# Kernel optimization log

Measured on AMD Instinct MI355X. Metric: run time of the kernel, lower is better.

Reference implementation:

```python
import math
import jax, jax.numpy as jnp
import numpy as np

N_EMBD = 1024
N_HEAD = 16
HEAD_DIM = N_EMBD // N_HEAD
B, T = 4, 2048
LN_EPS = 1e-5


def setup_inputs() -> dict:
    key = jax.random.key(0)
    ks = jax.random.split(key, 20)
    s = 0.02
    d = {
        'x': jax.random.normal(ks[0], (B, T, N_EMBD), jnp.float32),
        'Wq': jax.random.normal(ks[1], (N_EMBD, N_EMBD), jnp.float32) * s,
        'bq': jnp.zeros((N_EMBD,), jnp.float32),
        'Wk': jax.random.normal(ks[2], (N_EMBD, N_EMBD), jnp.float32) * s,
        'bk': jnp.zeros((N_EMBD,), jnp.float32),
        'Wv': jax.random.normal(ks[3], (N_EMBD, N_EMBD), jnp.float32) * s,
        'bv': jnp.zeros((N_EMBD,), jnp.float32),
        'Wo': jax.random.normal(ks[4], (N_EMBD, N_EMBD), jnp.float32) * s,
        'bo': jnp.zeros((N_EMBD,), jnp.float32),
        'ln1_g': jnp.ones((N_EMBD,), jnp.float32),
        'ln1_b': jnp.zeros((N_EMBD,), jnp.float32),
        'ln2_g': jnp.ones((N_EMBD,), jnp.float32),
        'ln2_b': jnp.zeros((N_EMBD,), jnp.float32),
        'W_fc': jax.random.normal(ks[5], (N_EMBD, 4 * N_EMBD), jnp.float32) * s,
        'b_fc': jnp.zeros((4 * N_EMBD,), jnp.float32),
        'W_proj': jax.random.normal(ks[6], (4 * N_EMBD, N_EMBD), jnp.float32) * s,
        'b_proj': jnp.zeros((N_EMBD,), jnp.float32),
    }
    return d


def _layernorm(x, g, b):
    mu = jnp.mean(x, axis=-1, keepdims=True)
    var = jnp.var(x, axis=-1, keepdims=True)
    return (x - mu) * jax.lax.rsqrt(var + LN_EPS) * g + b


def _new_gelu(x):
    c = math.sqrt(2.0 / math.pi)
    return 0.5 * x * (1.0 + jnp.tanh(c * (x + 0.044715 * x ** 3)))


def _attn(x, Wq, bq, Wk, bk, Wv, bv, Wo, bo):
    Bq, Tq, C = x.shape
    def heads(y):  # (B,T,C) -> (B,H,T,D)
        return y.reshape(Bq, Tq, N_HEAD, HEAD_DIM).transpose(0, 2, 1, 3)
    q = heads(x @ Wq + bq)
    k = heads(x @ Wk + bk)
    v = heads(x @ Wv + bv)
    scores = jnp.einsum('bhqd,bhkd->bhqk', q, k) / math.sqrt(HEAD_DIM)
    causal = jnp.tril(jnp.ones((Tq, Tq), bool))
    scores = jnp.where(causal, scores, -jnp.inf)
    w = jax.nn.softmax(scores, axis=-1)
    av = jnp.einsum('bhqk,bhkd->bhqd', w, v)
    av = av.transpose(0, 2, 1, 3).reshape(Bq, Tq, C)
    return av @ Wo + bo


def reference(x, Wq, bq, Wk, bk, Wv, bv, Wo, bo, ln1_g, ln1_b, ln2_g, ln2_b, W_fc, b_fc, W_proj, b_proj):
    x = x + _attn(_layernorm(x, ln1_g, ln1_b), Wq, bq, Wk, bk, Wv, bv, Wo, bo)
    h = _layernorm(x, ln2_g, ln2_b)
    x = x + (_new_gelu(h @ W_fc + b_fc) @ W_proj + b_proj)
    return x
```

## Files before the change

### kernel.cpp

```cpp
#include <hip/hip_runtime.h>

typedef __attribute__((ext_vector_type(8))) short short8;
typedef __attribute__((ext_vector_type(4))) short short4v;
typedef __attribute__((ext_vector_type(4))) float floatx4;
typedef unsigned short u16;

#define MFMA16(a,b,c) __builtin_amdgcn_mfma_f32_16x16x32_bf16(a,b,c,0,0,0)

typedef const __attribute__((address_space(1))) void* gas1;
typedef __attribute__((address_space(3))) void* las3;
static __device__ __forceinline__ void glds16(const void* g, void* l){
  __builtin_amdgcn_global_load_lds((gas1)g, (las3)l, 16, 0, 0);
}

static __device__ __forceinline__ u16 f2b(float f){
  union { float f; unsigned int u; } c; c.f = f;
  unsigned int u = c.u;
  u += 0x7fffu + ((u >> 16) & 1u);
  return (u16)(u >> 16);
}

static __device__ __forceinline__ unsigned int cvtpk(float lo, float hi){
  unsigned int r;
  asm("v_cvt_pk_bf16_f32 %0, %1, %2" : "=v"(r) : "v"(lo), "v"(hi));
  return r;
}

__global__ __launch_bounds__(256) void prep_kernel(
    const float* __restrict__ Wq, const float* __restrict__ Wk,
    const float* __restrict__ Wv, const float* __restrict__ Wo,
    const float* __restrict__ Wfc, const float* __restrict__ Wpj,
    u16* __restrict__ Wqkvt, u16* __restrict__ Wot,
    u16* __restrict__ Wfct, u16* __restrict__ Wpjt,
    const float* __restrict__ bq, const float* __restrict__ bk,
    const float* __restrict__ bv, float* __restrict__ bqkv)
{
  const int id = blockIdx.x;
  if (id == 12288){
    for (int i = threadIdx.x; i < 3072; i += 256)
      bqkv[i] = i < 1024 ? bq[i] : (i < 2048 ? bk[i - 1024] : bv[i - 2048]);
    return;
  }
  const float* W; u16* Wt; int K, N, loc, tshift;
  if (id < 4096){
    K = 1024; N = 1024; loc = id & 1023; tshift = 5;
    const int w = id >> 10;
    W  = (w == 0) ? Wq : (w == 1) ? Wk : (w == 2) ? Wv : Wo;
    Wt = (w == 3) ? Wot : Wqkvt + (size_t)w * 1024 * 1024;
  } else if (id < 8192){
    K = 1024; N = 4096; loc = id - 4096; tshift = 7; W = Wfc; Wt = Wfct;
  } else {
    K = 4096; N = 1024; loc = id - 8192; tshift = 5; W = Wpj; Wt = Wpjt;
  }
  const int nx = (loc & ((1 << tshift) - 1)) * 32;
  const int kx = (loc >> tshift) * 32;
  __shared__ float tile[32][33];
  const int tx = threadIdx.x & 31, ty = threadIdx.x >> 5;
  #pragma unroll
  for (int i = ty; i < 32; i += 8)
    tile[i][tx] = W[(size_t)(kx + i) * N + nx + tx];
  __syncthreads();
  #pragma unroll
  for (int i = ty; i < 32; i += 8)
    Wt[(size_t)(nx + i) * K + kx + tx] = f2b(tile[tx][i]);
}

__global__ __launch_bounds__(256) void ln_kernel(
    const float* __restrict__ x, const float* __restrict__ g,
    const float* __restrict__ b, u16* __restrict__ out){
  const int row = blockIdx.x, tid = threadIdx.x;
  const float4 v = reinterpret_cast<const float4*>(x + (size_t)row * 1024)[tid];
  float s  = v.x + v.y + v.z + v.w;
  float s2 = v.x*v.x + v.y*v.y + v.z*v.z + v.w*v.w;
  #pragma unroll
  for (int off = 1; off < 64; off <<= 1){
    s  += __shfl_xor(s,  off);
    s2 += __shfl_xor(s2, off);
  }
  __shared__ float red[8];
  const int wave = tid >> 6, lane = tid & 63;
  if (lane == 0){ red[wave] = s; red[4 + wave] = s2; }
  __syncthreads();
  s  = red[0] + red[1] + red[2] + red[3];
  s2 = red[4] + red[5] + red[6] + red[7];
  const float mu  = s * (1.f/1024.f);
  const float var = s2 * (1.f/1024.f) - mu * mu;
  const float rs  = rsqrtf(var + 1e-5f);
  const float4 gg = reinterpret_cast<const float4*>(g)[tid];
  const float4 bb = reinterpret_cast<const float4*>(b)[tid];
  ushort4 o;
  o.x = f2b((v.x - mu) * rs * gg.x + bb.x);
  o.y = f2b((v.y - mu) * rs * gg.y + bb.y);
  o.z = f2b((v.z - mu) * rs * gg.z + bb.z);
  o.w = f2b((v.w - mu) * rs * gg.w + bb.w);
  reinterpret_cast<ushort4*>(out + (size_t)row * 1024)[tid] = o;
}

template<bool GELU, bool RES, bool OUTBF, bool QKVMODE>
__global__ __launch_bounds__(256) void gemm128(
    const u16* __restrict__ A, const u16* __restrict__ Bt,
    const float* __restrict__ bias,
    const float* __restrict__ res,
    float* __restrict__ outF, u16* __restrict__ outB,
    u16* __restrict__ vtb,
    int M, int N, int K)
{
  __shared__ __attribute__((aligned(16))) u16 sA[2][128 * 32];
  __shared__ __attribute__((aligned(16))) u16 sB[2][128 * 32];
  const int tid  = threadIdx.x;
  const int wave = tid >> 6, lane = tid & 63, quad = lane >> 4, l16 = lane & 15;
  const int m0 = blockIdx.x * 128, n0 = blockIdx.y * 128;
  const int wm = (wave >> 1) * 64, wn = (wave & 1) * 64;

  const int scol = ((lane & 3) ^ ((lane >> 3) & 3)) * 8;
  const size_t aoff  = (size_t)(m0 + wave*32 + (lane >> 2)) * K + scol;
  const size_t aoff2 = aoff + (size_t)16 * K;
  const int brow = n0 + (wave >> 1)*64 + 4*(lane >> 2) + (wave & 1)*2;
  const size_t boff  = (size_t)brow * K + scol;
  const size_t boff2 = boff + (size_t)K;
  u16* alp = sA[0] + wave * 1024;
  u16* blp = sB[0] + wave * 1024;
  const int qx = (quad ^ ((l16 >> 1) & 3)) * 8;

  floatx4 acc[4][4];
  #pragma unroll
  for (int i = 0; i < 4; i++)
    #pragma unroll
    for (int nt = 0; nt < 4; nt++) acc[i][nt] = floatx4{0.f,0.f,0.f,0.f};

  glds16(A  + aoff,  alp);
  glds16(A  + aoff2, alp + 512);
  glds16(Bt + boff,  blp);
  glds16(Bt + boff2, blp + 512);

  int buf = 0;
  for (int k0 = 0; k0 < K; k0 += 32, buf ^= 1){
    __syncthreads();
    if (k0 + 32 < K){
      const int kn = k0 + 32;
      const int bo = (buf ^ 1) * 4096;
      glds16(A  + aoff  + kn, alp + bo);
      glds16(A  + aoff2 + kn, alp + bo + 512);
      glds16(Bt + boff  + kn, blp + bo);
      glds16(Bt + boff2 + kn, blp + bo + 512);
    }
    const u16* sa = sA[buf];
    const u16* sb = sB[buf];
    short8 af[4], bf[4];
    #pragma unroll
    for (int i = 0; i < 4; i++)
      af[i] = *reinterpret_cast<const short8*>(&sa[(wm + i*16 + l16)*32 + qx]);
    #pragma unroll
    for (int nt = 0; nt < 4; nt++)
      bf[nt] = *reinterpret_cast<const short8*>(&sb[(wn + nt*16 + l16)*32 + qx]);
    #pragma unroll
    for (int i = 0; i < 4; i++)
      #pragma unroll
      for (int nt = 0; nt < 4; nt++)
        acc[i][nt] = MFMA16(af[i], bf[nt], acc[i][nt]);
  }

  const int col0 = n0 + wn + 4*l16;
  const floatx4 bi = *reinterpret_cast<const floatx4*>(&bias[col0]);

  if (QKVMODE && n0 >= 2048){
    #pragma unroll
    for (int nt = 0; nt < 4; nt++){
      const int hd = col0 + nt - 2048;
      u16* vcol = vtb + (size_t)(hd >> 6) * 131072 + (size_t)(hd & 63) * 2048;
      #pragma unroll
      for (int i = 0; i < 4; i++){
        const int t0 = m0 + wm + i*16 + quad*4;
        const int bb = t0 >> 11, tt = t0 & 2047;
        short4v pk;
        #pragma unroll
        for (int r = 0; r < 4; r++) pk[r] = (short)f2b(acc[i][nt][r] + bi[nt]);
        *reinterpret_cast<short4v*>(vcol + (size_t)bb * 2097152 + tt) = pk;
      }
    }
    return;
  }

  #pragma unroll
  for (int i = 0; i < 4; i++){
    #pragma unroll
    for (int r = 0; r < 4; r++){
      const int row = m0 + wm + i*16 + quad*4 + r;
      if (OUTBF){
        short4v o;
        #pragma unroll
        for (int nt = 0; nt < 4; nt++){
          float val = acc[i][nt][r] + bi[nt];
          if (GELU){
            const float t = 0.7978845608028654f * (val + 0.044715f * val * val * val);
            val = val / (1.f + __expf(-2.f * t));
          }
          o[nt] = (short)f2b(val);
        }
        *reinterpret_cast<short4v*>(&outB[(size_t)row * N + col0]) = o;
      } else {
        floatx4 v;
        #pragma unroll
        for (int nt = 0; nt < 4; nt++) v[nt] = acc[i][nt][r] + bi[nt];
        if (RES){
          const floatx4 rr = *reinterpret_cast<const floatx4*>(&res[(size_t)row * N + col0]);
          #pragma unroll
          for (int nt = 0; nt < 4; nt++) v[nt] += rr[nt];
        }
        *reinterpret_cast<floatx4*>(&outF[(size_t)row * N + col0]) = v;
      }
    }
  }
}

__global__ __launch_bounds__(256) void attn_kernel(
    const u16* __restrict__ qkv, const u16* __restrict__ vtb,
    u16* __restrict__ O)
{
  constexpr int T = 2048, LDQ = 3072, LDP = 72;
  constexpr float CE = 0.18033688011112042f;
  __shared__ __attribute__((aligned(16))) u16 sK[2][2][64*32];
  __shared__ __attribute__((aligned(16))) u16 sV[2][2][64*32];
  __shared__ __attribute__((aligned(16))) u16 sP[4][16*LDP];

  const int tid = threadIdx.x, wave = tid >> 6, lane = tid & 63;
  const int quad = lane >> 4, l16 = lane & 15;

  const int lin = blockIdx.y * 16 + blockIdx.x;
  const int j = lin & 15;
  const int bh = lin >> 4;
  const int kk4 = bh >> 4;
  const int jj = (j + ((kk4 & 2) << 2)) & 15;
  const int qt = (kk4 & 1) ? (15 - jj) : jj;
  const int q0 = qt * 128;
  const int b = bh >> 4, h = bh & 15;

  const u16* Qp = qkv + (size_t)b * T * LDQ + h * 64;
  const u16* Kp = Qp + 1024;
  const u16* Vt = vtb + (size_t)bh * 64 * T;

  const int qx = (quad ^ ((l16 >> 1) & 3)) * 8;

  int qg[2]; qg[0] = q0 + wave*16 + l16; qg[1] = qg[0] + 64;
  short8 qf[2][2];
  #pragma unroll
  for (int g = 0; g < 2; g++){
    qf[g][0] = *reinterpret_cast<const short8*>(&Qp[(size_t)qg[g]*LDQ + quad*8]);
    qf[g][1] = *reinterpret_cast<const short8*>(&Qp[(size_t)qg[g]*LDQ + 32 + quad*8]);
  }

  float m_i[2] = {-INFINITY, -INFINITY}, l_i[2] = {0.f, 0.f};
  floatx4 o_acc[2][4];
  #pragma unroll
  for (int g = 0; g < 2; g++)
    #pragma unroll
    for (int nt = 0; nt < 4; nt++) o_acc[g][nt] = floatx4{0.f,0.f,0.f,0.f};

  const int srow = wave*16 + (lane >> 2);
  const int scol = ((lane & 3) ^ ((lane >> 3) & 3)) * 8;
  const int asrc = (lane & 48) | (quad * 4);

  const int kend = q0 + 128;

  {
    glds16(Kp + (size_t)srow*LDQ + scol,      sK[0][0] + wave*512);
    glds16(Kp + (size_t)srow*LDQ + 32 + scol, sK[0][1] + wave*512);
    glds16(Vt + (size_t)srow*T + scol,        sV[0][0] + wave*512);
    glds16(Vt + (size_t)srow*T + 32 + scol,   sV[0][1] + wave*512);
  }

  int buf = 0;
  for (int k0 = 0; k0 < kend; k0 += 64, buf ^= 1){
    __syncthreads();
    if (k0 + 64 < kend){
      const int kn = k0 + 64;
      glds16(Kp + (size_t)(kn + srow)*LDQ + scol,      sK[buf^1][0] + wave*512);
      glds16(Kp + (size_t)(kn + srow)*LDQ + 32 + scol, sK[buf^1][1] + wave*512);
      glds16(Vt + (size_t)srow*T + kn + scol,          sV[buf^1][0] + wave*512);
      glds16(Vt + (size_t)srow*T + kn + 32 + scol,     sV[buf^1][1] + wave*512);
    }

    #pragma unroll
    for (int g = 0; g < 2; g++){
      if (g == 0 && k0 > q0) continue;

      float s[4][4];
      __builtin_amdgcn_s_setprio(1);
      #pragma unroll
      for (int sub = 0; sub < 4; sub++){
        floatx4 sa = floatx4{0.f,0.f,0.f,0.f};
        const short8 kf0 = *reinterpret_cast<const short8*>(&sK[buf][0][(sub*16 + l16)*32 + qx]);
        const short8 kf1 = *reinterpret_cast<const short8*>(&sK[buf][1][(sub*16 + l16)*32 + qx]);
        sa = MFMA16(kf0, qf[g][0], sa);
        sa = MFMA16(kf1, qf[g][1], sa);
        #pragma unroll
        for (int r = 0; r < 4; r++) s[sub][r] = sa[r];
      }
      __builtin_amdgcn_s_setprio(0);
      if (k0 == q0 + g*64){
        #pragma unroll
        for (int sub = 0; sub < 4; sub++)
          #pragma unroll
          for (int r = 0; r < 4; r++){
            const int kidx = k0 + sub*16 + quad*4 + r;
            if (kidx > qg[g]) s[sub][r] = -1e30f;
          }
      }

      float sm[4];
      #pragma unroll
      for (int sub = 0; sub < 4; sub++)
        sm[sub] = fmaxf(fmaxf(s[sub][0], s[sub][1]), fmaxf(s[sub][2], s[sub][3]));
      float mx = fmaxf(fmaxf(sm[0], sm[1]), fmaxf(sm[2], sm[3]));
      mx = fmaxf(mx, __shfl_xor(mx, 16));
      mx = fmaxf(mx, __shfl_xor(mx, 32));

      const bool up = mx > m_i[g] + 32.f;
      const float mnew = up ? mx : m_i[g];

      float p[4][4], rs[4];
      #pragma unroll
      for (int sub = 0; sub < 4; sub++){
        #pragma unroll
        for (int r = 0; r < 4; r++)
          p[sub][r] = __builtin_amdgcn_exp2f(CE * (s[sub][r] - mnew));
        rs[sub] = (p[sub][0] + p[sub][1]) + (p[sub][2] + p[sub][3]);
      }
      float rowsum = (rs[0] + rs[1]) + (rs[2] + rs[3]);
      rowsum += __shfl_xor(rowsum, 16);
      rowsum += __shfl_xor(rowsum, 32);

      if (__any(up)){
        const float alpha = up ? __builtin_amdgcn_exp2f(CE * (m_i[g] - mnew)) : 1.f;
        float arow[4];
        #pragma unroll
        for (int r = 0; r < 4; r++) arow[r] = __shfl(alpha, asrc + r);
        #pragma unroll
        for (int nt = 0; nt < 4; nt++)
          #pragma unroll
          for (int r = 0; r < 4; r++) o_acc[g][nt][r] *= arow[r];
        l_i[g] *= alpha;
        m_i[g] = mnew;
      }
      l_i[g] += rowsum;

      #pragma unroll
      for (int sub = 0; sub < 4; sub++){
        uint2 pk2;
        pk2.x = cvtpk(p[sub][0], p[sub][1]);
        pk2.y = cvtpk(p[sub][2], p[sub][3]);
        *reinterpret_cast<uint2*>(&sP[wave][l16*LDP + sub*16 + quad*4]) = pk2;
      }
      const short8 pf0 = *reinterpret_cast<const short8*>(&sP[wave][l16*LDP + quad*8]);
      const short8 pf1 = *reinterpret_cast<const short8*>(&sP[wave][l16*LDP + 32 + quad*8]);
      __builtin_amdgcn_s_setprio(1);
      #pragma unroll
      for (int nt = 0; nt < 4; nt++){
        const short8 vf0 = *reinterpret_cast<const short8*>(&sV[buf][0][(nt*16 + l16)*32 + qx]);
        const short8 vf1 = *reinterpret_cast<const short8*>(&sV[buf][1][(nt*16 + l16)*32 + qx]);
        o_acc[g][nt] = MFMA16(pf0, vf0, o_acc[g][nt]);
        o_acc[g][nt] = MFMA16(pf1, vf1, o_acc[g][nt]);
      }
      __builtin_amdgcn_s_setprio(0);
    }
  }

  #pragma unroll
  for (int g = 0; g < 2; g++){
    float lrow[4];
    #pragma unroll
    for (int r = 0; r < 4; r++) lrow[r] = __shfl(l_i[g], asrc + r);
    #pragma unroll
    for (int nt = 0; nt < 4; nt++){
      #pragma unroll
      for (int r = 0; r < 4; r++){
        const int row = q0 + g*64 + wave*16 + quad*4 + r;
        O[(size_t)(b*T + row)*1024 + h*64 + nt*16 + l16] = f2b(o_acc[g][nt][r] / lrow[r]);
      }
    }
  }
}

extern "C" void kernel_launch(void* const* d_in, const int* in_sizes, int n_in,
                              void* d_out, int out_size, void* d_ws, size_t ws_size,
                              hipStream_t stream){
  const float* x      = (const float*)d_in[0];
  const float* Wq     = (const float*)d_in[1];
  const float* bq     = (const float*)d_in[2];
  const float* Wk     = (const float*)d_in[3];
  const float* bk     = (const float*)d_in[4];
  const float* Wv     = (const float*)d_in[5];
  const float* bv     = (const float*)d_in[6];
  const float* Wo     = (const float*)d_in[7];
  const float* bo     = (const float*)d_in[8];
  const float* ln1_g  = (const float*)d_in[9];
  const float* ln1_b  = (const float*)d_in[10];
  const float* ln2_g  = (const float*)d_in[11];
  const float* ln2_b  = (const float*)d_in[12];
  const float* W_fc   = (const float*)d_in[13];
  const float* b_fc   = (const float*)d_in[14];
  const float* W_proj = (const float*)d_in[15];
  const float* b_proj = (const float*)d_in[16];
  float* out = (float*)d_out;
  char* ws = (char*)d_ws;
  const size_t MB = 1024 * 1024;

  u16* bufA  = (u16*)(ws);
  u16* qkvb  = (u16*)(ws + 16*MB);
  u16* vtb   = (u16*)(ws + 64*MB);
  u16* fcb   = (u16*)(ws + 16*MB);
  float* x2  = out;
  u16* Wqkvt = (u16*)(ws + 80*MB);
  u16* Wot   = (u16*)(ws + 86*MB);
  u16* Wfct  = (u16*)(ws + 88*MB);
  u16* Wpjt  = (u16*)(ws + 96*MB);
  float* bqkv= (float*)(ws + 104*MB);

  dim3 tb(256);
  prep_kernel<<<dim3(12289), tb, 0, stream>>>(
      Wq, Wk, Wv, Wo, W_fc, W_proj, Wqkvt, Wot, Wfct, Wpjt, bq, bk, bv, bqkv);

  ln_kernel<<<8192, tb, 0, stream>>>(x, ln1_g, ln1_b, bufA);

  gemm128<false,false,true,true><<<dim3(64,24), tb, 0, stream>>>(
      bufA, Wqkvt, bqkv, nullptr, nullptr, qkvb, vtb, 8192, 3072, 1024);

  attn_kernel<<<dim3(16, 64), tb, 0, stream>>>(qkvb, vtb, bufA);

  gemm128<false,true,false,false><<<dim3(64,8), tb, 0, stream>>>(
      bufA, Wot, bo, x, x2, nullptr, nullptr, 8192, 1024, 1024);

  ln_kernel<<<8192, tb, 0, stream>>>(x2, ln2_g, ln2_b, bufA);

  gemm128<true,false,true,false><<<dim3(64,32), tb, 0, stream>>>(
      bufA, Wfct, b_fc, nullptr, nullptr, fcb, nullptr, 8192, 4096, 1024);

  gemm128<false,true,false,false><<<dim3(64,8), tb, 0, stream>>>(
      fcb, Wpjt, b_proj, x2, out, nullptr, nullptr, 8192, 1024, 4096);
}
```

Measured before the change: 532.7 us.

## Fold softmax scale into Q projection and interleave two query groups in attention

The QKV GEMM epilogue now multiplies Q outputs by the log2e/sqrt(d) constant, so the attention kernel's exp2 drops its per-element multiply. The attention inner loop processes both 64-row query groups in one pass, sharing K/V fragment loads and interleaving MFMAs, and uses a per-lane lazy max check that only rescales when some lane's max rises by more than 4 (in log2 units). Block-to-(batch,head,qtile) mapping is changed too. This trades more registers and a second P buffer for fewer LDS reads and fewer warp-wide shuffles in the common case.

After: 545.7 us. 2.4% more time.

```diff
diff --git a/kernel.cpp b/kernel.cpp
--- a/kernel.cpp
+++ b/kernel.cpp
@@ -162,6 +162,7 @@
 
   const int col0 = n0 + wn + 4*l16;
   const floatx4 bi = *reinterpret_cast<const floatx4*>(&bias[col0]);
+  const float qsc = (QKVMODE && n0 < 1024) ? 0.18033688011112042f : 1.f;
 
   if (QKVMODE && n0 >= 2048){
     #pragma unroll
@@ -195,6 +196,7 @@
             const float t = 0.7978845608028654f * (val + 0.044715f * val * val * val);
             val = val / (1.f + __expf(-2.f * t));
           }
+          if (QKVMODE) val *= qsc;
           o[nt] = (short)f2b(val);
         }
         *reinterpret_cast<short4v*>(&outB[(size_t)row * N + col0]) = o;
@@ -218,20 +220,18 @@
     u16* __restrict__ O)
 {
   constexpr int T = 2048, LDQ = 3072, LDP = 72;
-  constexpr float CE = 0.18033688011112042f;
   __shared__ __attribute__((aligned(16))) u16 sK[2][2][64*32];
   __shared__ __attribute__((aligned(16))) u16 sV[2][2][64*32];
-  __shared__ __attribute__((aligned(16))) u16 sP[4][16*LDP];
+  __shared__ __attribute__((aligned(16))) u16 sP[4][2][16*LDP];
 
   const int tid = threadIdx.x, wave = tid >> 6, lane = tid & 63;
   const int quad = lane >> 4, l16 = lane & 15;
 
-  const int lin = blockIdx.y * 16 + blockIdx.x;
-  const int j = lin & 15;
-  const int bh = lin >> 4;
-  const int kk4 = bh >> 4;
-  const int jj = (j + ((kk4 & 2) << 2)) & 15;
-  const int qt = (kk4 & 1) ? (15 - jj) : jj;
+  const int d  = blockIdx.y * 16 + blockIdx.x;
+  const int r_ = d >> 3;
+  const int hg = r_ >> 4, jj = r_ & 15;
+  const int bh = (d & 7) * 8 + hg;
+  const int qt = (hg & 2) ? (15 - jj) : jj;
   const int q0 = qt * 128;
   const int b = bh >> 4, h = bh & 15;
 
@@ -268,6 +268,48 @@
     glds16(Vt + (size_t)srow*T + scol,        sV[0][0] + wave*512);
     glds16(Vt + (size_t)srow*T + 32 + scol,   sV[0][1] + wave*512);
   }
+
+#define SMSTEP(S_, P_, G_) do { \
+    const float mo_ = m_i[G_]; \
+    _Pragma("unroll") \
+    for (int su_ = 0; su_ < 4; su_++) \
+      _Pragma("unroll") \
+      for (int rr_ = 0; rr_ < 4; rr_++) \
+        P_[su_][rr_] = __builtin_amdgcn_exp2f(S_[su_][rr_] - mo_); \
+    float t0_ = fmaxf(fmaxf(S_[0][0],S_[0][1]), fmaxf(S_[0][2],S_[0][3])); \
+    float t1_ = fmaxf(fmaxf(S_[1][0],S_[1][1]), fmaxf(S_[1][2],S_[1][3])); \
+    float t2_ = fmaxf(fmaxf(S_[2][0],S_[2][1]), fmaxf(S_[2][2],S_[2][3])); \
+    float t3_ = fmaxf(fmaxf(S_[3][0],S_[3][1]), fmaxf(S_[3][2],S_[3][3])); \
+    float mx_ = fmaxf(fmaxf(t0_,t1_), fmaxf(t2_,t3_)); \
+    if (__builtin_expect(__any(mx_ > mo_ + 4.f), 0)){ \
+      mx_ = fmaxf(mx_, __shfl_xor(mx_, 16)); \
+      mx_ = fmaxf(mx_, __shfl_xor(mx_, 32)); \
+      const float mn_ = fmaxf(mo_, mx_); \
+      const float al_ = __builtin_amdgcn_exp2f(mo_ - mn_); \
+      _Pragma("unroll") \
+      for (int su_ = 0; su_ < 4; su_++) \
+        _Pragma("unroll") \
+        for (int rr_ = 0; rr_ < 4; rr_++) \
+          P_[su_][rr_] = __builtin_amdgcn_exp2f(S_[su_][rr_] - mn_); \
+      float ar_[4]; \
+      _Pragma("unroll") \
+      for (int rr_ = 0; rr_ < 4; rr_++) ar_[rr_] = __shfl(al_, asrc + rr_); \
+      _Pragma("unroll") \
+      for (int nt_ = 0; nt_ < 4; nt_++) \
+        _Pragma("unroll") \
+        for (int rr_ = 0; rr_ < 4; rr_++) o_acc[G_][nt_][rr_] *= ar_[rr_]; \
+      l_i[G_] *= al_; \
+      m_i[G_] = mn_; \
+    } \
+    float rA_ = (P_[0][0]+P_[0][1]) + (P_[0][2]+P_[0][3]); \
+    float rB_ = (P_[1][0]+P_[1][1]) + (P_[1][2]+P_[1][3]); \
+    float rC_ = (P_[2][0]+P_[2][1]) + (P_[2][2]+P_[2][3]); \
+    float rD_ = (P_[3][0]+P_[3][1]) + (P_[3][2]+P_[3][3]); \
+    float rw_ = (rA_+rB_) + (rC_+rD_); \
+    rw_ += __shfl_xor(rw_, 16); \
+    rw_ += __shfl_xor(rw_, 32); \
+    l_i[G_] += rw_; \
+  } while(0)
 
   int buf = 0;
   for (int k0 = 0; k0 < kend; k0 += 64, buf ^= 1){
@@ -280,102 +322,97 @@
       glds16(Vt + (size_t)srow*T + kn + 32 + scol,     sV[buf^1][1] + wave*512);
     }
 
-    #pragma unroll
-    for (int g = 0; g < 2; g++){
-      if (g == 0 && k0 > q0) continue;
-
-      float s[4][4];
-      __builtin_amdgcn_s_setprio(1);
-      #pragma unroll
-      for (int sub = 0; sub < 4; sub++){
-        floatx4 sa = floatx4{0.f,0.f,0.f,0.f};
-        const short8 kf0 = *reinterpret_cast<const short8*>(&sK[buf][0][(sub*16 + l16)*32 + qx]);
-        const short8 kf1 = *reinterpret_cast<const short8*>(&sK[buf][1][(sub*16 + l16)*32 + qx]);
-        sa = MFMA16(kf0, qf[g][0], sa);
-        sa = MFMA16(kf1, qf[g][1], sa);
-        #pragma unroll
-        for (int r = 0; r < 4; r++) s[sub][r] = sa[r];
-      }
-      __builtin_amdgcn_s_setprio(0);
-      if (k0 == q0 + g*64){
-        #pragma unroll
-        for (int sub = 0; sub < 4; sub++)
-          #pragma unroll
-          for (int r = 0; r < 4; r++){
-            const int kidx = k0 + sub*16 + quad*4 + r;
-            if (kidx > qg[g]) s[sub][r] = -1e30f;
-          }
-      }
-
-      float sm[4];
+    const bool g0act = (k0 <= q0);
+
+    float s0[4][4], s1[4][4];
+    __builtin_amdgcn_s_setprio(1);
+    #pragma unroll
+    for (int sub = 0; sub < 4; sub++){
+      const short8 kf0 = *reinterpret_cast<const short8*>(&sK[buf][0][(sub*16 + l16)*32 + qx]);
+      const short8 kf1 = *reinterpret_cast<const short8*>(&sK[buf][1][(sub*16 + l16)*32 + qx]);
+      floatx4 sa1 = MFMA16(kf0, qf[1][0], (floatx4{0.f,0.f,0.f,0.f}));
+      sa1 = MFMA16(kf1, qf[1][1], sa1);
+      #pragma unroll
+      for (int r2 = 0; r2 < 4; r2++) s1[sub][r2] = sa1[r2];
+      if (g0act){
+        floatx4 sa0 = MFMA16(kf0, qf[0][0], (floatx4{0.f,0.f,0.f,0.f}));
+        sa0 = MFMA16(kf1, qf[0][1], sa0);
+        #pragma unroll
+        for (int r2 = 0; r2 < 4; r2++) s0[sub][r2] = sa0[r2];
+      }
+    }
+    __builtin_amdgcn_s_setprio(0);
+
+    if (k0 == q0){
       #pragma unroll
       for (int sub = 0; sub < 4; sub++)
-        sm[sub] = fmaxf(fmaxf(s[sub][0], s[sub][1]), fmaxf(s[sub][2], s[sub][3]));
-      float mx = fmaxf(fmaxf(sm[0], sm[1]), fmaxf(sm[2], sm[3]));
-      mx = fmaxf(mx, __shfl_xor(mx, 16));
-      mx = fmaxf(mx, __shfl_xor(mx, 32));
-
-      const bool up = mx > m_i[g] + 32.f;
-      const float mnew = up ? mx : m_i[g];
-
-      float p[4][4], rs[4];
-      #pragma unroll
-      for (int sub = 0; sub < 4; sub++){
-        #pragma unroll
-        for (int r = 0; r < 4; r++)
-          p[sub][r] = __builtin_amdgcn_exp2f(CE * (s[sub][r] - mnew));
-        rs[sub] = (p[sub][0] + p[sub][1]) + (p[sub][2] + p[sub][3]);
-      }
-      float rowsum = (rs[0] + rs[1]) + (rs[2] + rs[3]);
-      rowsum += __shfl_xor(rowsum, 16);
-      rowsum += __shfl_xor(rowsum, 32);
-
-      if (__any(up)){
-        const float alpha = up ? __builtin_amdgcn_exp2f(CE * (m_i[g] - mnew)) : 1.f;
-        float arow[4];
-        #pragma unroll
-        for (int r = 0; r < 4; r++) arow[r] = __shfl(alpha, asrc + r);
-        #pragma unroll
-        for (int nt = 0; nt < 4; nt++)
-          #pragma unroll
-          for (int r = 0; r < 4; r++) o_acc[g][nt][r] *= arow[r];
-        l_i[g] *= alpha;
-        m_i[g] = mnew;
-      }
-      l_i[g] += rowsum;
-
+        #pragma unroll
+        for (int r2 = 0; r2 < 4; r2++)
+          if (k0 + sub*16 + quad*4 + r2 > qg[0]) s0[sub][r2] = -1e30f;
+    }
+    if (k0 == q0 + 64){
+      #pragma unroll
+      for (int sub = 0; sub < 4; sub++)
+        #pragma unroll
+        for (int r2 = 0; r2 < 4; r2++)
+          if (k0 + sub*16 + quad*4 + r2 > qg[1]) s1[sub][r2] = -1e30f;
+    }
+
+    float p0[4][4], p1[4][4];
+    if (g0act) SMSTEP(s0, p0, 0);
+    SMSTEP(s1, p1, 1);
+
+    if (g0act){
       #pragma unroll
       for (int sub = 0; sub < 4; sub++){
         uint2 pk2;
-        pk2.x = cvtpk(p[sub][0], p[sub][1]);
-        pk2.y = cvtpk(p[sub][2], p[sub][3]);
-        *reinterpret_cast<uint2*>(&sP[wave][l16*LDP + sub*16 + quad*4]) = pk2;
-      }
-      const short8 pf0 = *reinterpret_cast<const short8*>(&sP[wave][l16*LDP + quad*8]);
-      const short8 pf1 = *reinterpret_cast<const short8*>(&sP[wave][l16*LDP + 32 + quad*8]);
-      __builtin_amdgcn_s_setprio(1);
-      #pragma unroll
-      for (int nt = 0; nt < 4; nt++){
-        const short8 vf0 = *reinterpret_cast<const short8*>(&sV[buf][0][(nt*16 + l16)*32 + qx]);
-        const short8 vf1 = *reinterpret_cast<const short8*>(&sV[buf][1][(nt*16 + l16)*32 + qx]);
-        o_acc[g][nt] = MFMA16(pf0, vf0, o_acc[g][nt]);
-        o_acc[g][nt] = MFMA16(pf1, vf1, o_acc[g][nt]);
-      }
-      __builtin_amdgcn_s_setprio(0);
-    }
-  }
+        pk2.x = cvtpk(p0[sub][0], p0[sub][1]);
+        pk2.y = cvtpk(p0[sub][2], p0[sub][3]);
+        *reinterpret_cast<uint2*>(&sP[wave][0][l16*LDP + sub*16 + quad*4]) = pk2;
+      }
+    }
+    #pragma unroll
+    for (int sub = 0; sub < 4; sub++){
+      uint2 pk2;
+      pk2.x = cvtpk(p1[sub][0], p1[sub][1]);
+      pk2.y = cvtpk(p1[sub][2], p1[sub][3]);
+      *reinterpret_cast<uint2*>(&sP[wave][1][l16*LDP + sub*16 + quad*4]) = pk2;
+    }
+    short8 pf00, pf01;
+    if (g0act){
+      pf00 = *reinterpret_cast<const short8*>(&sP[wave][0][l16*LDP + quad*8]);
+      pf01 = *reinterpret_cast<const short8*>(&sP[wave][0][l16*LDP + 32 + quad*8]);
+    }
+    const short8 pf10 = *reinterpret_cast<const short8*>(&sP[wave][1][l16*LDP + quad*8]);
+    const short8 pf11 = *reinterpret_cast<const short8*>(&sP[wave][1][l16*LDP + 32 + quad*8]);
+
+    __builtin_amdgcn_s_setprio(1);
+    #pragma unroll
+    for (int nt = 0; nt < 4; nt++){
+      const short8 vf0 = *reinterpret_cast<const short8*>(&sV[buf][0][(nt*16 + l16)*32 + qx]);
+      const short8 vf1 = *reinterpret_cast<const short8*>(&sV[buf][1][(nt*16 + l16)*32 + qx]);
+      if (g0act){
+        o_acc[0][nt] = MFMA16(pf00, vf0, o_acc[0][nt]);
+        o_acc[0][nt] = MFMA16(pf01, vf1, o_acc[0][nt]);
+      }
+      o_acc[1][nt] = MFMA16(pf10, vf0, o_acc[1][nt]);
+      o_acc[1][nt] = MFMA16(pf11, vf1, o_acc[1][nt]);
+    }
+    __builtin_amdgcn_s_setprio(0);
+  }
+#undef SMSTEP
 
   #pragma unroll
   for (int g = 0; g < 2; g++){
     float lrow[4];
     #pragma unroll
-    for (int r = 0; r < 4; r++) lrow[r] = __shfl(l_i[g], asrc + r);
+    for (int r2 = 0; r2 < 4; r2++) lrow[r2] = __shfl(l_i[g], asrc + r2);
     #pragma unroll
     for (int nt = 0; nt < 4; nt++){
       #pragma unroll
-      for (int r = 0; r < 4; r++){
-        const int row = q0 + g*64 + wave*16 + quad*4 + r;
-        O[(size_t)(b*T + row)*1024 + h*64 + nt*16 + l16] = f2b(o_acc[g][nt][r] / lrow[r]);
+      for (int r2 = 0; r2 < 4; r2++){
+        const int row = q0 + g*64 + wave*16 + quad*4 + r2;
+        O[(size_t)(b*T + row)*1024 + h*64 + nt*16 + l16] = f2b(o_acc[g][nt][r2] / lrow[r2]);
       }
     }
   }
```

## Split attention query tile across eight waves and fold softmax scale into Q

Applied to the files above, without the earlier changes.

The attention kernel moves from 4 waves that each handle two 16-row query groups to 8 waves that each handle one group. The K/V tile loads are split so that waves 0-3 load K and waves 4-7 load V. The softmax scale times log2(e) is folded into Q inside the QKV GEMM epilogue, which removes a multiply per score element. The lazy-rescale threshold changes to match the new base-2 units. The block-to-head mapping is also reordered, and launch bounds are raised to 512 threads. The aim is more parallelism and less per-wave serial work on the causal diagonal, at the cost of more waves per block and a different block schedule.

Measured after the change: 522.2 us. 1.02x faster.

```diff
diff --git a/kernel.cpp b/kernel.cpp
--- a/kernel.cpp
+++ b/kernel.cpp
@@ -162,6 +162,7 @@
 
   const int col0 = n0 + wn + 4*l16;
   const floatx4 bi = *reinterpret_cast<const floatx4*>(&bias[col0]);
+  const float qsc = (QKVMODE && n0 < 1024) ? 0.18033688011112042f : 1.f;
 
   if (QKVMODE && n0 >= 2048){
     #pragma unroll
@@ -195,6 +196,7 @@
             const float t = 0.7978845608028654f * (val + 0.044715f * val * val * val);
             val = val / (1.f + __expf(-2.f * t));
           }
+          if (QKVMODE) val *= qsc;
           o[nt] = (short)f2b(val);
         }
         *reinterpret_cast<short4v*>(&outB[(size_t)row * N + col0]) = o;
@@ -213,25 +215,23 @@
   }
 }
 
-__global__ __launch_bounds__(256) void attn_kernel(
+__global__ __launch_bounds__(512, 6) void attn_kernel(
     const u16* __restrict__ qkv, const u16* __restrict__ vtb,
     u16* __restrict__ O)
 {
   constexpr int T = 2048, LDQ = 3072, LDP = 72;
-  constexpr float CE = 0.18033688011112042f;
   __shared__ __attribute__((aligned(16))) u16 sK[2][2][64*32];
   __shared__ __attribute__((aligned(16))) u16 sV[2][2][64*32];
-  __shared__ __attribute__((aligned(16))) u16 sP[4][16*LDP];
+  __shared__ __attribute__((aligned(16))) u16 sP[8][16*LDP];
 
   const int tid = threadIdx.x, wave = tid >> 6, lane = tid & 63;
   const int quad = lane >> 4, l16 = lane & 15;
 
-  const int lin = blockIdx.y * 16 + blockIdx.x;
-  const int j = lin & 15;
-  const int bh = lin >> 4;
-  const int kk4 = bh >> 4;
-  const int jj = (j + ((kk4 & 2) << 2)) & 15;
-  const int qt = (kk4 & 1) ? (15 - jj) : jj;
+  const int d  = blockIdx.y * 16 + blockIdx.x;
+  const int r_ = d >> 3;
+  const int hg = r_ >> 4, jj = r_ & 15;
+  const int bh = (d & 7) * 8 + hg;
+  const int qt = (hg & 2) ? (15 - jj) : jj;
   const int q0 = qt * 128;
   const int b = bh >> 4, h = bh & 15;
 
@@ -241,142 +241,133 @@
 
   const int qx = (quad ^ ((l16 >> 1) & 3)) * 8;
 
-  int qg[2]; qg[0] = q0 + wave*16 + l16; qg[1] = qg[0] + 64;
-  short8 qf[2][2];
-  #pragma unroll
-  for (int g = 0; g < 2; g++){
-    qf[g][0] = *reinterpret_cast<const short8*>(&Qp[(size_t)qg[g]*LDQ + quad*8]);
-    qf[g][1] = *reinterpret_cast<const short8*>(&Qp[(size_t)qg[g]*LDQ + 32 + quad*8]);
-  }
-
-  float m_i[2] = {-INFINITY, -INFINITY}, l_i[2] = {0.f, 0.f};
-  floatx4 o_acc[2][4];
-  #pragma unroll
-  for (int g = 0; g < 2; g++)
-    #pragma unroll
-    for (int nt = 0; nt < 4; nt++) o_acc[g][nt] = floatx4{0.f,0.f,0.f,0.f};
-
-  const int srow = wave*16 + (lane >> 2);
+  const int kq = q0 + wave * 16;
+  const int qg = kq + l16;
+  const short8 qf0 = *reinterpret_cast<const short8*>(&Qp[(size_t)qg*LDQ + quad*8]);
+  const short8 qf1 = *reinterpret_cast<const short8*>(&Qp[(size_t)qg*LDQ + 32 + quad*8]);
+
+  float m_i = -INFINITY, l_i = 0.f;
+  floatx4 o_acc[4];
+  #pragma unroll
+  for (int nt = 0; nt < 4; nt++) o_acc[nt] = floatx4{0.f,0.f,0.f,0.f};
+
+  const int sw = wave & 3;
+  const int srow = sw*16 + (lane >> 2);
   const int scol = ((lane & 3) ^ ((lane >> 3) & 3)) * 8;
+  const bool isK = wave < 4;
+  const u16* g0 = isK ? (Kp + (size_t)srow*LDQ + scol) : (Vt + (size_t)srow*T + scol);
+  const u16* g1 = g0 + 32;
+  const size_t gs = isK ? (size_t)LDQ : (size_t)1;
+  u16* l0 = (isK ? &sK[0][0][0] : &sV[0][0][0]) + sw*512;
+  u16* l1 = (isK ? &sK[0][1][0] : &sV[0][1][0]) + sw*512;
+
+  glds16(g0, l0);
+  glds16(g1, l1);
+
   const int asrc = (lane & 48) | (quad * 4);
-
   const int kend = q0 + 128;
-
-  {
-    glds16(Kp + (size_t)srow*LDQ + scol,      sK[0][0] + wave*512);
-    glds16(Kp + (size_t)srow*LDQ + 32 + scol, sK[0][1] + wave*512);
-    glds16(Vt + (size_t)srow*T + scol,        sV[0][0] + wave*512);
-    glds16(Vt + (size_t)srow*T + 32 + scol,   sV[0][1] + wave*512);
-  }
 
   int buf = 0;
   for (int k0 = 0; k0 < kend; k0 += 64, buf ^= 1){
     __syncthreads();
     if (k0 + 64 < kend){
-      const int kn = k0 + 64;
-      glds16(Kp + (size_t)(kn + srow)*LDQ + scol,      sK[buf^1][0] + wave*512);
-      glds16(Kp + (size_t)(kn + srow)*LDQ + 32 + scol, sK[buf^1][1] + wave*512);
-      glds16(Vt + (size_t)srow*T + kn + scol,          sV[buf^1][0] + wave*512);
-      glds16(Vt + (size_t)srow*T + kn + 32 + scol,     sV[buf^1][1] + wave*512);
-    }
-
-    #pragma unroll
-    for (int g = 0; g < 2; g++){
-      if (g == 0 && k0 > q0) continue;
-
+      const size_t adv = (size_t)(k0 + 64) * gs;
+      glds16(g0 + adv, l0 + (buf ^ 1) * 4096);
+      glds16(g1 + adv, l1 + (buf ^ 1) * 4096);
+    }
+
+    if (k0 <= kq + 15){
       float s[4][4];
       __builtin_amdgcn_s_setprio(1);
       #pragma unroll
       for (int sub = 0; sub < 4; sub++){
-        floatx4 sa = floatx4{0.f,0.f,0.f,0.f};
         const short8 kf0 = *reinterpret_cast<const short8*>(&sK[buf][0][(sub*16 + l16)*32 + qx]);
         const short8 kf1 = *reinterpret_cast<const short8*>(&sK[buf][1][(sub*16 + l16)*32 + qx]);
-        sa = MFMA16(kf0, qf[g][0], sa);
-        sa = MFMA16(kf1, qf[g][1], sa);
+        floatx4 sa = MFMA16(kf0, qf0, (floatx4{0.f,0.f,0.f,0.f}));
+        sa = MFMA16(kf1, qf1, sa);
         #pragma unroll
         for (int r = 0; r < 4; r++) s[sub][r] = sa[r];
       }
       __builtin_amdgcn_s_setprio(0);
-      if (k0 == q0 + g*64){
+
+      if (k0 + 63 > kq){
         #pragma unroll
         for (int sub = 0; sub < 4; sub++)
           #pragma unroll
-          for (int r = 0; r < 4; r++){
-            const int kidx = k0 + sub*16 + quad*4 + r;
-            if (kidx > qg[g]) s[sub][r] = -1e30f;
-          }
-      }
-
-      float sm[4];
-      #pragma unroll
-      for (int sub = 0; sub < 4; sub++)
-        sm[sub] = fmaxf(fmaxf(s[sub][0], s[sub][1]), fmaxf(s[sub][2], s[sub][3]));
-      float mx = fmaxf(fmaxf(sm[0], sm[1]), fmaxf(sm[2], sm[3]));
+          for (int r = 0; r < 4; r++)
+            if (k0 + sub*16 + quad*4 + r > qg) s[sub][r] = -1e30f;
+      }
+
+      float t0 = fmaxf(fmaxf(s[0][0],s[0][1]), fmaxf(s[0][2],s[0][3]));
+      float t1 = fmaxf(fmaxf(s[1][0],s[1][1]), fmaxf(s[1][2],s[1][3]));
+      float t2 = fmaxf(fmaxf(s[2][0],s[2][1]), fmaxf(s[2][2],s[2][3]));
+      float t3 = fmaxf(fmaxf(s[3][0],s[3][1]), fmaxf(s[3][2],s[3][3]));
+      float mx = fmaxf(fmaxf(t0,t1), fmaxf(t2,t3));
       mx = fmaxf(mx, __shfl_xor(mx, 16));
       mx = fmaxf(mx, __shfl_xor(mx, 32));
 
-      const bool up = mx > m_i[g] + 32.f;
-      const float mnew = up ? mx : m_i[g];
-
-      float p[4][4], rs[4];
-      #pragma unroll
-      for (int sub = 0; sub < 4; sub++){
+      const bool up = mx > m_i + 6.f;
+      const float mnew = up ? mx : m_i;
+
+      #pragma unroll
+      for (int sub = 0; sub < 4; sub++)
         #pragma unroll
         for (int r = 0; r < 4; r++)
-          p[sub][r] = __builtin_amdgcn_exp2f(CE * (s[sub][r] - mnew));
-        rs[sub] = (p[sub][0] + p[sub][1]) + (p[sub][2] + p[sub][3]);
-      }
-      float rowsum = (rs[0] + rs[1]) + (rs[2] + rs[3]);
+          s[sub][r] = __builtin_amdgcn_exp2f(s[sub][r] - mnew);
+
+      float rA = (s[0][0]+s[0][1]) + (s[0][2]+s[0][3]);
+      float rB = (s[1][0]+s[1][1]) + (s[1][2]+s[1][3]);
+      float rC = (s[2][0]+s[2][1]) + (s[2][2]+s[2][3]);
+      float rD = (s[3][0]+s[3][1]) + (s[3][2]+s[3][3]);
+      float rowsum = (rA+rB) + (rC+rD);
       rowsum += __shfl_xor(rowsum, 16);
       rowsum += __shfl_xor(rowsum, 32);
 
       if (__any(up)){
-        const float alpha = up ? __builtin_amdgcn_exp2f(CE * (m_i[g] - mnew)) : 1.f;
+        const float alpha = up ? __builtin_amdgcn_exp2f(m_i - mnew) : 1.f;
         float arow[4];
         #pragma unroll
         for (int r = 0; r < 4; r++) arow[r] = __shfl(alpha, asrc + r);
         #pragma unroll
         for (int nt = 0; nt < 4; nt++)
           #pragma unroll
-          for (int r = 0; r < 4; r++) o_acc[g][nt][r] *= arow[r];
-        l_i[g] *= alpha;
-        m_i[g] = mnew;
-      }
-      l_i[g] += rowsum;
+          for (int r = 0; r < 4; r++) o_acc[nt][r] *= arow[r];
+        l_i *= alpha;
+        m_i = mnew;
+      }
+      l_i += rowsum;
 
       #pragma unroll
       for (int sub = 0; sub < 4; sub++){
         uint2 pk2;
-        pk2.x = cvtpk(p[sub][0], p[sub][1]);
-        pk2.y = cvtpk(p[sub][2], p[sub][3]);
+        pk2.x = cvtpk(s[sub][0], s[sub][1]);
+        pk2.y = cvtpk(s[sub][2], s[sub][3]);
         *reinterpret_cast<uint2*>(&sP[wave][l16*LDP + sub*16 + quad*4]) = pk2;
       }
       const short8 pf0 = *reinterpret_cast<const short8*>(&sP[wave][l16*LDP + quad*8]);
       const short8 pf1 = *reinterpret_cast<const short8*>(&sP[wave][l16*LDP + 32 + quad*8]);
+
       __builtin_amdgcn_s_setprio(1);
       #pragma unroll
       for (int nt = 0; nt < 4; nt++){
         const short8 vf0 = *reinterpret_cast<const short8*>(&sV[buf][0][(nt*16 + l16)*32 + qx]);
         const short8 vf1 = *reinterpret_cast<const short8*>(&sV[buf][1][(nt*16 + l16)*32 + qx]);
-        o_acc[g][nt] = MFMA16(pf0, vf0, o_acc[g][nt]);
-        o_acc[g][nt] = MFMA16(pf1, vf1, o_acc[g][nt]);
+        o_acc[nt] = MFMA16(pf0, vf0, o_acc[nt]);
+        o_acc[nt] = MFMA16(pf1, vf1, o_acc[nt]);
       }
       __builtin_amdgcn_s_setprio(0);
     }
   }
 
-  #pragma unroll
-  for (int g = 0; g < 2; g++){
-    float lrow[4];
-    #pragma unroll
-    for (int r = 0; r < 4; r++) lrow[r] = __shfl(l_i[g], asrc + r);
-    #pragma unroll
-    for (int nt = 0; nt < 4; nt++){
-      #pragma unroll
-      for (int r = 0; r < 4; r++){
-        const int row = q0 + g*64 + wave*16 + quad*4 + r;
-        O[(size_t)(b*T + row)*1024 + h*64 + nt*16 + l16] = f2b(o_acc[g][nt][r] / lrow[r]);
-      }
+  float lrow[4];
+  #pragma unroll
+  for (int r = 0; r < 4; r++) lrow[r] = __shfl(l_i, asrc + r);
+  #pragma unroll
+  for (int nt = 0; nt < 4; nt++){
+    #pragma unroll
+    for (int r = 0; r < 4; r++){
+      const int row = kq + quad*4 + r;
+      O[(size_t)(b*T + row)*1024 + h*64 + nt*16 + l16] = f2b(o_acc[nt][r] / lrow[r]);
     }
   }
 }
@@ -425,7 +416,7 @@
   gemm128<false,false,true,true><<<dim3(64,24), tb, 0, stream>>>(
       bufA, Wqkvt, bqkv, nullptr, nullptr, qkvb, vtb, 8192, 3072, 1024);
 
-  attn_kernel<<<dim3(16, 64), tb, 0, stream>>>(qkvb, vtb, bufA);
+  attn_kernel<<<dim3(16, 64), dim3(512), 0, stream>>>(qkvb, vtb, bufA);
 
   gemm128<false,true,false,false><<<dim3(64,8), tb, 0, stream>>>(
       bufA, Wot, bo, x, x2, nullptr, nullptr, 8192, 1024, 1024);
```
